# Optimization experiments

Measured on AMD Instinct MI355X. Metric: run time of the kernel, lower is better.

The kernel has to match this reference:

```python
import jax, jax.numpy as jnp
import numpy as np

NUM_NEURONS = 2048
EMBED_DIM = 1024
WINDOW_SIZES = np.array([1, 2, 4, 8, 16, 32, 64, 128, 256, 512, 1024, 2048], dtype=np.int32)
WINDOW_MAX = 2048
TEMPERATURE = 1.0


def setup_inputs() -> dict:
    key = jax.random.key(0)
    ks = jax.random.split(key, 12)
    W = len(WINDOW_SIZES)
    inp = {
        "x": jax.random.normal(ks[0], (8192, EMBED_DIM), dtype=jnp.float32),
        "n_weights": jax.random.normal(ks[1], (NUM_NEURONS, EMBED_DIM), dtype=jnp.float32) * 0.01,
        "n_biases": jnp.zeros((NUM_NEURONS,), dtype=jnp.float32),
        "combo_w": jax.random.normal(ks[2], (W, NUM_NEURONS, NUM_NEURONS), dtype=jnp.float32) * (1.0 / np.sqrt(NUM_NEURONS)),
        "combo_b": jax.random.normal(ks[3], (W, NUM_NEURONS), dtype=jnp.float32) * 0.01,
        "q_w": jax.random.normal(ks[4], (EMBED_DIM, NUM_NEURONS), dtype=jnp.float32) * (1.0 / np.sqrt(NUM_NEURONS)),
        "q_b": jnp.zeros((EMBED_DIM,), dtype=jnp.float32),
        "k_w": jax.random.normal(ks[5], (EMBED_DIM, NUM_NEURONS), dtype=jnp.float32) * (1.0 / np.sqrt(NUM_NEURONS)),
        "k_b": jnp.zeros((EMBED_DIM,), dtype=jnp.float32),
        "cerebellum": jnp.ones((W,), dtype=jnp.float32),
        "judge_bias": jnp.zeros((W,), dtype=jnp.float32),
        "credibility_bias": jnp.zeros((W,), dtype=jnp.float32),
        "parliament_blend": jnp.float32(0.5),
    }
    return inp


def _forward(x, n_weights, n_biases, combo_w, combo_b, q_w, q_b, k_w, k_b,
             cerebellum, judge_bias, credibility_bias, parliament_blend):
    # NEURON forward: [S, E] @ [E, N] + [N] -> tanh -> clamp
    act = jnp.clip(jnp.tanh(x @ n_weights.T + n_biases), -5.0, 5.0)  # [S, N]
    S = act.shape[0]
    tail = min(S, WINDOW_MAX)
    # faithful replication of stackedWindowMeans: last `tail` activations go to the
    # END of a [WINDOW_MAX, N] buffer, mask selects the FIRST windowSize rows
    padded = jnp.zeros((WINDOW_MAX, NUM_NEURONS), dtype=act.dtype).at[WINDOW_MAX - tail:].set(act[S - tail:])
    wsz = jnp.asarray(WINDOW_SIZES, dtype=jnp.float32)  # [W]
    mask = (jnp.arange(WINDOW_MAX)[None, :] < jnp.asarray(WINDOW_SIZES)[:, None]).astype(act.dtype)  # [W, WINDOW_MAX]
    window_out = (mask @ padded) / wsz[:, None]  # [W, N]
    # per-window Linear combos (torch Linear: y = x @ W.T + b)
    combo = jnp.einsum('wn,wmn->wm', window_out, combo_w) + combo_b  # [W, N]
    query = combo @ q_w.T + q_b + (judge_bias * cerebellum)[:, None]  # [W, E]
    key = window_out @ k_w.T + k_b + (credibility_bias * cerebellum)[:, None]  # [W, E]
    scores = (query @ key.T) / TEMPERATURE  # [W, W]
    # selfScores + peerScores == column sums of scores
    combined_scores = scores.sum(axis=0)  # [W]
    pb = jax.nn.sigmoid(parliament_blend)
    blended = ((1.0 - pb) * cerebellum + pb * combined_scores) * cerebellum
    combined_window_weights = jax.nn.softmax(blended)  # [W]
    ctx = jnp.sum(combo + combined_window_weights[:, None], axis=0, keepdims=True)  # [1, N]
    ctx = ctx + 0.2 * combo.mean(axis=0, keepdims=True)
    return ctx


def reference(x, n_weights, n_biases, combo_w, combo_b, q_w, q_b, k_w, k_b,
              cerebellum, judge_bias, credibility_bias, parliament_blend):
    return _forward(x, n_weights, n_biases, combo_w, combo_b, q_w, q_b, k_w, k_b,
                    cerebellum, judge_bias, credibility_bias, parliament_blend)
```

## Files before the change

### kernel.cpp

```cpp
#include <hip/hip_runtime.h>
#include <hip/hip_bf16.h>
#include <math.h>

#define N_NEUR 2048
#define EMB 1024
#define S_TOT 8192
#define NW 12

typedef __attribute__((ext_vector_type(8))) short bf16x8;
typedef __attribute__((ext_vector_type(4))) float f32x4;

__device__ inline short f2bf(float f) {
    union { float f; unsigned u; } v; v.f = f;
    unsigned r = v.u + 0x7FFFu + ((v.u >> 16) & 1u);
    return (short)(r >> 16);
}

__global__ __launch_bounds__(256) void precast(const float* __restrict__ xt,
                                               const float* __restrict__ nw,
                                               short* __restrict__ A,
                                               short* __restrict__ W,
                                               float* __restrict__ seg) {
    const int HALF = (N_NEUR * EMB) / 4;
    int g = blockIdx.x * 256 + threadIdx.x;
    if (g < (NW * N_NEUR) / 4) ((float4*)seg)[g] = make_float4(0.f, 0.f, 0.f, 0.f);
    int gg = g;
    const float4* src; short* dst;
    if (gg < HALF) { src = (const float4*)xt; dst = A; }
    else           { gg -= HALF; src = (const float4*)nw; dst = W; }
    float4 v = src[gg];
    short4 o;
    o.x = f2bf(v.x); o.y = f2bf(v.y); o.z = f2bf(v.z); o.w = f2bf(v.w);
    *(short4*)(dst + (size_t)gg * 4) = o;
}

#define GLDS(g, l) __builtin_amdgcn_global_load_lds(                          \
    (const __attribute__((address_space(1))) void*)(g),                       \
    (__attribute__((address_space(3))) void*)(l), 16, 0, 0)

__global__ __launch_bounds__(256) void gemm_seg(const short* __restrict__ A,
                                                const short* __restrict__ W,
                                                const float* __restrict__ bias,
                                                float* __restrict__ seg) {
    __shared__ short As[2][64 * 64];
    __shared__ short Bs[2][64 * 64];
    const int t = threadIdx.x;
    const int bm = blockIdx.y, bn = blockIdx.x;
    const int lane = t & 63, wid = t >> 6;
    const int wr = wid >> 1, wc = wid & 1;
    const int l15 = lane & 15, lhi = lane >> 4;
    const int srow = lane >> 3;
    const int pslot = (lane & 7) ^ srow;
    const short* gA0 = A + (size_t)(bm * 64 + wid * 16 + 0 + srow) * EMB + pslot * 8;
    const short* gA1 = A + (size_t)(bm * 64 + wid * 16 + 8 + srow) * EMB + pslot * 8;
    const short* gB0 = W + (size_t)(bn * 64 + wid * 16 + 0 + srow) * EMB + pslot * 8;
    const short* gB1 = W + (size_t)(bn * 64 + wid * 16 + 8 + srow) * EMB + pslot * 8;
    short* lA0[2] = { &As[0][(wid * 16 + 0) * 64], &As[1][(wid * 16 + 0) * 64] };
    short* lA1[2] = { &As[0][(wid * 16 + 8) * 64], &As[1][(wid * 16 + 8) * 64] };
    short* lB0[2] = { &Bs[0][(wid * 16 + 0) * 64], &Bs[1][(wid * 16 + 0) * 64] };
    short* lB1[2] = { &Bs[0][(wid * 16 + 8) * 64], &Bs[1][(wid * 16 + 8) * 64] };

    f32x4 acc[2][2] = {};

    GLDS(gA0, lA0[0]); GLDS(gA1, lA1[0]);
    GLDS(gB0, lB0[0]); GLDS(gB1, lB1[0]);
    __syncthreads();

    int cur = 0;
    for (int ks = 0; ks < 16; ++ks) {
        if (ks < 15) {
            int k0 = (ks + 1) * 64;
            GLDS(gA0 + k0, lA0[cur ^ 1]); GLDS(gA1 + k0, lA1[cur ^ 1]);
            GLDS(gB0 + k0, lB0[cur ^ 1]); GLDS(gB1 + k0, lB1[cur ^ 1]);
        }
        bf16x8 af[2][2], bb[2][2];
        #pragma unroll
        for (int kk = 0; kk < 2; ++kk) {
            #pragma unroll
            for (int m = 0; m < 2; ++m) {
                int row = wr * 32 + m * 16 + l15;
                int slot = (kk * 4 + lhi) ^ (row & 7);
                af[kk][m] = *(const bf16x8*)&As[cur][row * 64 + slot * 8];
            }
            #pragma unroll
            for (int n = 0; n < 2; ++n) {
                int row = wc * 32 + n * 16 + l15;
                int slot = (kk * 4 + lhi) ^ (row & 7);
                bb[kk][n] = *(const bf16x8*)&Bs[cur][row * 64 + slot * 8];
            }
        }
        __builtin_amdgcn_s_setprio(1);
        #pragma unroll
        for (int kk = 0; kk < 2; ++kk)
            #pragma unroll
            for (int m = 0; m < 2; ++m)
                #pragma unroll
                for (int n = 0; n < 2; ++n)
                    acc[m][n] = __builtin_amdgcn_mfma_f32_16x16x32_bf16(af[kk][m], bb[kk][n], acc[m][n], 0, 0, 0);
        __builtin_amdgcn_s_setprio(0);
        __syncthreads();
        cur ^= 1;
    }

    if (bm > 0) {
        int jseg = 38 - __clz(bm);
        #pragma unroll
        for (int n = 0; n < 2; ++n) {
            int col = bn * 64 + wc * 32 + n * 16 + l15;
            float bc = bias[col];
            float s = 0.f;
            #pragma unroll
            for (int m = 0; m < 2; ++m)
                #pragma unroll
                for (int j = 0; j < 4; ++j)
                    s += tanhf(acc[m][n][j] + bc);
            s += __shfl_xor(s, 16);
            s += __shfl_xor(s, 32);
            if (lhi == 0) atomicAdd(&seg[jseg * N_NEUR + col], s);
        }
    } else {
        #pragma unroll
        for (int n = 0; n < 2; ++n) {
            int col = bn * 64 + wc * 32 + n * 16 + l15;
            float bc = bias[col];
            if (wr == 1) {
                float s = 0.f;
                #pragma unroll
                for (int m = 0; m < 2; ++m)
                    #pragma unroll
                    for (int j = 0; j < 4; ++j)
                        s += tanhf(acc[m][n][j] + bc);
                s += __shfl_xor(s, 16);
                s += __shfl_xor(s, 32);
                if (lhi == 0) atomicAdd(&seg[6 * N_NEUR + col], s);
            } else {
                float s = 0.f;
                #pragma unroll
                for (int j = 0; j < 4; ++j)
                    s += tanhf(acc[1][n][j] + bc);
                s += __shfl_xor(s, 16);
                s += __shfl_xor(s, 32);
                if (lhi == 0) atomicAdd(&seg[5 * N_NEUR + col], s);
                #pragma unroll
                for (int j = 0; j < 4; ++j) {
                    int r = lhi * 4 + j;
                    int sj = (r == 0) ? 0 : (32 - __clz(r));
                    atomicAdd(&seg[sj * N_NEUR + col], tanhf(acc[0][n][j] + bc));
                }
            }
        }
    }
}

__global__ __launch_bounds__(256) void winout_init(const float* __restrict__ seg,
                                                   const float* __restrict__ cb,
                                                   float* __restrict__ wout,
                                                   float* __restrict__ out) {
    int n = blockIdx.x * 256 + threadIdx.x;
    float run = 0.f;
    #pragma unroll
    for (int w = 0; w < NW; ++w) {
        run += seg[w * N_NEUR + n];
        wout[w * N_NEUR + n] = run * (1.0f / (float)(1 << w));
    }
    float bs = 0.f;
    #pragma unroll
    for (int w = 0; w < NW; ++w) bs += cb[w * N_NEUR + n];
    out[n] = 1.0166666666666666f * bs + 1.0f;
}

__global__ __launch_bounds__(256) void combo_dot(const float* __restrict__ cw,
                                                 const float* __restrict__ wout,
                                                 float* __restrict__ out) {
    int wid = threadIdx.x >> 6, lane = threadIdx.x & 63;
    int r = blockIdx.x * 4 + wid;
    int w = r >> 11, m = r & 2047;
    const float4* row  = (const float4*)(cw + (size_t)(w * N_NEUR + m) * N_NEUR);
    const float4* wrow = (const float4*)(wout + w * N_NEUR);
    float s = 0.f;
    #pragma unroll
    for (int i = 0; i < 8; ++i) {
        float4 a = row[i * 64 + lane];
        float4 b = wrow[i * 64 + lane];
        s += a.x * b.x + a.y * b.y + a.z * b.z + a.w * b.w;
    }
    #pragma unroll
    for (int off = 32; off > 0; off >>= 1) s += __shfl_down(s, off);
    if (lane == 0) atomicAdd(&out[m], 1.0166666666666666f * s);
}

extern "C" void kernel_launch(void* const* d_in, const int* in_sizes, int n_in,
                              void* d_out, int out_size, void* d_ws, size_t ws_size,
                              hipStream_t stream) {
    const float* x  = (const float*)d_in[0];
    const float* nw = (const float*)d_in[1];
    const float* nb = (const float*)d_in[2];
    const float* cw = (const float*)d_in[3];
    const float* cb = (const float*)d_in[4];
    float* out = (float*)d_out;

    char* ws = (char*)d_ws;
    float* seg  = (float*)ws;
    float* wout = (float*)(ws + 98304);
    short* Abf  = (short*)(ws + 204800);
    short* Wbf  = (short*)(ws + 204800 + 4194304);

    precast<<<4096, 256, 0, stream>>>(x + (size_t)(S_TOT - 2048) * EMB, nw, Abf, Wbf, seg);

    dim3 g1(32, 32);
    gemm_seg<<<g1, 256, 0, stream>>>(Abf, Wbf, nb, seg);

    winout_init<<<8, 256, 0, stream>>>(seg, cb, wout, out);

    combo_dot<<<6144, 256, 0, stream>>>(cw, wout, out);
}
```

Before: 57.03 us.

## Triple-buffer GEMM LDS pipeline and remap blocks for XCD-local tile reuse

The bf16 GEMM main loop moves from double to triple buffering. It prefetches two K-steps ahead and uses explicit vmcnt waits plus a single barrier per iteration in place of two syncthreads. The grid becomes 1D with a swizzle that gives each XCD a contiguous 16x8 block of output tiles, which should improve L2 reuse of the A and B panels. This costs more LDS per block, which can reduce occupancy, and it relies on hand-tuned waitcnt values being correct.

```diff
diff --git a/kernel.cpp b/kernel.cpp
--- a/kernel.cpp
+++ b/kernel.cpp
@@ -42,10 +42,13 @@
                                                 const short* __restrict__ W,
                                                 const float* __restrict__ bias,
                                                 float* __restrict__ seg) {
-    __shared__ short As[2][64 * 64];
-    __shared__ short Bs[2][64 * 64];
+    __shared__ short As[3][64 * 64];
+    __shared__ short Bs[3][64 * 64];
     const int t = threadIdx.x;
-    const int bm = blockIdx.y, bn = blockIdx.x;
+    const int wgid = blockIdx.x;
+    const int xcd = wgid & 7, local = wgid >> 3;
+    const int bm = (xcd >> 2) * 16 + (local >> 3);
+    const int bn = (xcd & 3) * 8 + (local & 7);
     const int lane = t & 63, wid = t >> 6;
     const int wr = wid >> 1, wc = wid & 1;
     const int l15 = lane & 15, lhi = lane >> 4;
@@ -55,24 +58,34 @@
     const short* gA1 = A + (size_t)(bm * 64 + wid * 16 + 8 + srow) * EMB + pslot * 8;
     const short* gB0 = W + (size_t)(bn * 64 + wid * 16 + 0 + srow) * EMB + pslot * 8;
     const short* gB1 = W + (size_t)(bn * 64 + wid * 16 + 8 + srow) * EMB + pslot * 8;
-    short* lA0[2] = { &As[0][(wid * 16 + 0) * 64], &As[1][(wid * 16 + 0) * 64] };
-    short* lA1[2] = { &As[0][(wid * 16 + 8) * 64], &As[1][(wid * 16 + 8) * 64] };
-    short* lB0[2] = { &Bs[0][(wid * 16 + 0) * 64], &Bs[1][(wid * 16 + 0) * 64] };
-    short* lB1[2] = { &Bs[0][(wid * 16 + 8) * 64], &Bs[1][(wid * 16 + 8) * 64] };
+    short* baseA = &As[0][0];
+    short* baseB = &Bs[0][0];
+    const int aoff0 = (wid * 16 + 0) * 64;
+    const int aoff1 = (wid * 16 + 8) * 64;
+
+#define STAGE(b, k0) do {                                                     \
+    GLDS(gA0 + (k0), baseA + (b) * 4096 + aoff0);                             \
+    GLDS(gA1 + (k0), baseA + (b) * 4096 + aoff1);                             \
+    GLDS(gB0 + (k0), baseB + (b) * 4096 + aoff0);                             \
+    GLDS(gB1 + (k0), baseB + (b) * 4096 + aoff1);                             \
+    } while (0)
 
     f32x4 acc[2][2] = {};
 
-    GLDS(gA0, lA0[0]); GLDS(gA1, lA1[0]);
-    GLDS(gB0, lB0[0]); GLDS(gB1, lB1[0]);
-    __syncthreads();
-
-    int cur = 0;
+    STAGE(0, 0);
+    STAGE(1, 64);
+
+    int cur = 0, stg = 2;
     for (int ks = 0; ks < 16; ++ks) {
-        if (ks < 15) {
-            int k0 = (ks + 1) * 64;
-            GLDS(gA0 + k0, lA0[cur ^ 1]); GLDS(gA1 + k0, lA1[cur ^ 1]);
-            GLDS(gB0 + k0, lB0[cur ^ 1]); GLDS(gB1 + k0, lB1[cur ^ 1]);
-        }
+        if (ks < 15) asm volatile("s_waitcnt vmcnt(4)" ::: "memory");
+        else         asm volatile("s_waitcnt vmcnt(0)" ::: "memory");
+        __builtin_amdgcn_s_barrier();
+        if (ks + 2 < 16) {
+            STAGE(stg, (ks + 2) * 64);
+            stg = (stg == 2) ? 0 : stg + 1;
+        }
+        const short* rA = baseA + cur * 4096;
+        const short* rB = baseB + cur * 4096;
         bf16x8 af[2][2], bb[2][2];
         #pragma unroll
         for (int kk = 0; kk < 2; ++kk) {
@@ -80,13 +93,13 @@
             for (int m = 0; m < 2; ++m) {
                 int row = wr * 32 + m * 16 + l15;
                 int slot = (kk * 4 + lhi) ^ (row & 7);
-                af[kk][m] = *(const bf16x8*)&As[cur][row * 64 + slot * 8];
+                af[kk][m] = *(const bf16x8*)&rA[row * 64 + slot * 8];
             }
             #pragma unroll
             for (int n = 0; n < 2; ++n) {
                 int row = wc * 32 + n * 16 + l15;
                 int slot = (kk * 4 + lhi) ^ (row & 7);
-                bb[kk][n] = *(const bf16x8*)&Bs[cur][row * 64 + slot * 8];
+                bb[kk][n] = *(const bf16x8*)&rB[row * 64 + slot * 8];
             }
         }
         __builtin_amdgcn_s_setprio(1);
@@ -98,8 +111,7 @@
                 for (int n = 0; n < 2; ++n)
                     acc[m][n] = __builtin_amdgcn_mfma_f32_16x16x32_bf16(af[kk][m], bb[kk][n], acc[m][n], 0, 0, 0);
         __builtin_amdgcn_s_setprio(0);
-        __syncthreads();
-        cur ^= 1;
+        cur = (cur == 2) ? 0 : cur + 1;
     }
 
     if (bm > 0) {
@@ -207,8 +219,7 @@
 
     precast<<<4096, 256, 0, stream>>>(x + (size_t)(S_TOT - 2048) * EMB, nw, Abf, Wbf, seg);
 
-    dim3 g1(32, 32);
-    gemm_seg<<<g1, 256, 0, stream>>>(Abf, Wbf, nb, seg);
+    gemm_seg<<<1024, 256, 0, stream>>>(Abf, Wbf, nb, seg);
 
     winout_init<<<8, 256, 0, stream>>>(seg, cb, wout, out);
 
```

Result: slower. 65.47 us (+14.8%).

## Load GEMM B operand directly into registers instead of staging through LDS

Applied to the files above, without the earlier changes.

The neuron GEMM now fetches the weight (B) fragments straight from global memory into registers, double-buffered in two register sets across a manually unrolled k-loop, while A keeps the LDS global_load_lds path. This halves LDS usage and removes the LDS reads for B, and launch bounds now request 4 blocks per SM for higher occupancy. The cost is uncoalesced-ish 16-byte global loads per lane for B that are duplicated across the two warp rows, and more register pressure.

```diff
diff --git a/kernel.cpp b/kernel.cpp
--- a/kernel.cpp
+++ b/kernel.cpp
@@ -38,12 +38,11 @@
     (const __attribute__((address_space(1))) void*)(g),                       \
     (__attribute__((address_space(3))) void*)(l), 16, 0, 0)
 
-__global__ __launch_bounds__(256) void gemm_seg(const short* __restrict__ A,
-                                                const short* __restrict__ W,
-                                                const float* __restrict__ bias,
-                                                float* __restrict__ seg) {
+__global__ __launch_bounds__(256, 4) void gemm_seg(const short* __restrict__ A,
+                                                   const short* __restrict__ W,
+                                                   const float* __restrict__ bias,
+                                                   float* __restrict__ seg) {
     __shared__ short As[2][64 * 64];
-    __shared__ short Bs[2][64 * 64];
     const int t = threadIdx.x;
     const int bm = blockIdx.y, bn = blockIdx.x;
     const int lane = t & 63, wid = t >> 6;
@@ -53,53 +52,70 @@
     const int pslot = (lane & 7) ^ srow;
     const short* gA0 = A + (size_t)(bm * 64 + wid * 16 + 0 + srow) * EMB + pslot * 8;
     const short* gA1 = A + (size_t)(bm * 64 + wid * 16 + 8 + srow) * EMB + pslot * 8;
-    const short* gB0 = W + (size_t)(bn * 64 + wid * 16 + 0 + srow) * EMB + pslot * 8;
-    const short* gB1 = W + (size_t)(bn * 64 + wid * 16 + 8 + srow) * EMB + pslot * 8;
     short* lA0[2] = { &As[0][(wid * 16 + 0) * 64], &As[1][(wid * 16 + 0) * 64] };
     short* lA1[2] = { &As[0][(wid * 16 + 8) * 64], &As[1][(wid * 16 + 8) * 64] };
-    short* lB0[2] = { &Bs[0][(wid * 16 + 0) * 64], &Bs[1][(wid * 16 + 0) * 64] };
-    short* lB1[2] = { &Bs[0][(wid * 16 + 8) * 64], &Bs[1][(wid * 16 + 8) * 64] };
+    const short* gBn0 = W + (size_t)(bn * 64 + wc * 32 + 0 * 16 + l15) * EMB + lhi * 8;
+    const short* gBn1 = W + (size_t)(bn * 64 + wc * 32 + 1 * 16 + l15) * EMB + lhi * 8;
 
     f32x4 acc[2][2] = {};
 
+#define LOADB(dst, k0) do {                                                   \
+    dst[0][0] = *(const bf16x8*)(gBn0 + (k0));                                \
+    dst[1][0] = *(const bf16x8*)(gBn0 + (k0) + 32);                           \
+    dst[0][1] = *(const bf16x8*)(gBn1 + (k0));                                \
+    dst[1][1] = *(const bf16x8*)(gBn1 + (k0) + 32);                           \
+    } while (0)
+
+#define READA(buf)                                                            \
+    bf16x8 af[2][2];                                                          \
+    _Pragma("unroll")                                                         \
+    for (int kk = 0; kk < 2; ++kk)                                            \
+        _Pragma("unroll")                                                     \
+        for (int m = 0; m < 2; ++m) {                                         \
+            int row = wr * 32 + m * 16 + l15;                                 \
+            int slot = (kk * 4 + lhi) ^ (row & 7);                            \
+            af[kk][m] = *(const bf16x8*)&As[buf][row * 64 + slot * 8];        \
+        }
+
+#define DOMFMA(bsrc) do {                                                     \
+    __builtin_amdgcn_s_setprio(1);                                            \
+    _Pragma("unroll")                                                         \
+    for (int kk = 0; kk < 2; ++kk)                                            \
+        _Pragma("unroll")                                                     \
+        for (int m = 0; m < 2; ++m)                                           \
+            _Pragma("unroll")                                                 \
+            for (int n = 0; n < 2; ++n)                                       \
+                acc[m][n] = __builtin_amdgcn_mfma_f32_16x16x32_bf16(          \
+                    af[kk][m], bsrc[kk][n], acc[m][n], 0, 0, 0);              \
+    __builtin_amdgcn_s_setprio(0);                                            \
+    } while (0)
+
+    bf16x8 bregE[2][2], bregO[2][2];
+
     GLDS(gA0, lA0[0]); GLDS(gA1, lA1[0]);
-    GLDS(gB0, lB0[0]); GLDS(gB1, lB1[0]);
+    LOADB(bregE, 0);
     __syncthreads();
 
-    int cur = 0;
-    for (int ks = 0; ks < 16; ++ks) {
-        if (ks < 15) {
-            int k0 = (ks + 1) * 64;
-            GLDS(gA0 + k0, lA0[cur ^ 1]); GLDS(gA1 + k0, lA1[cur ^ 1]);
-            GLDS(gB0 + k0, lB0[cur ^ 1]); GLDS(gB1 + k0, lB1[cur ^ 1]);
-        }
-        bf16x8 af[2][2], bb[2][2];
-        #pragma unroll
-        for (int kk = 0; kk < 2; ++kk) {
-            #pragma unroll
-            for (int m = 0; m < 2; ++m) {
-                int row = wr * 32 + m * 16 + l15;
-                int slot = (kk * 4 + lhi) ^ (row & 7);
-                af[kk][m] = *(const bf16x8*)&As[cur][row * 64 + slot * 8];
+    #pragma unroll 1
+    for (int kp = 0; kp < 8; ++kp) {
+        {
+            int k0n = (2 * kp + 1) * 64;
+            GLDS(gA0 + k0n, lA0[1]); GLDS(gA1 + k0n, lA1[1]);
+            LOADB(bregO, k0n);
+            READA(0);
+            DOMFMA(bregE);
+            __syncthreads();
+        }
+        {
+            if (kp < 7) {
+                int k0n = (2 * kp + 2) * 64;
+                GLDS(gA0 + k0n, lA0[0]); GLDS(gA1 + k0n, lA1[0]);
+                LOADB(bregE, k0n);
             }
-            #pragma unroll
-            for (int n = 0; n < 2; ++n) {
-                int row = wc * 32 + n * 16 + l15;
-                int slot = (kk * 4 + lhi) ^ (row & 7);
-                bb[kk][n] = *(const bf16x8*)&Bs[cur][row * 64 + slot * 8];
-            }
-        }
-        __builtin_amdgcn_s_setprio(1);
-        #pragma unroll
-        for (int kk = 0; kk < 2; ++kk)
-            #pragma unroll
-            for (int m = 0; m < 2; ++m)
-                #pragma unroll
-                for (int n = 0; n < 2; ++n)
-                    acc[m][n] = __builtin_amdgcn_mfma_f32_16x16x32_bf16(af[kk][m], bb[kk][n], acc[m][n], 0, 0, 0);
-        __builtin_amdgcn_s_setprio(0);
-        __syncthreads();
-        cur ^= 1;
+            READA(1);
+            DOMFMA(bregO);
+            __syncthreads();
+        }
     }
 
     if (bm > 0) {
```

After: 78.06 us. 1.37x slower.
